# Kernel optimization log

Hardware: AMD Instinct MI355X
Metric: run time of the kernel (lower is better)

The kernel has to match this reference:

```python
import jax, jax.numpy as jnp
import numpy as np

B, S, HID, USZ, PSZ, OUT = 128, 512, 768, 200, 200, 200
N_SENT = 16  # 16 sentences of 32 tokens; offsets row = [0,32,...,480,-1]


def setup_inputs() -> dict:
    key = jax.random.key(0)
    ks = jax.random.split(key, 8)
    H = jax.random.normal(ks[0], (B, S, HID), jnp.float32)
    u = jax.random.normal(ks[1], (B, USZ), jnp.float32)
    p = jax.random.normal(ks[2], (B, PSZ), jnp.float32)
    Wh = jax.random.normal(ks[3], (HID, OUT), jnp.float32) * 0.05
    Wu = jax.random.normal(ks[4], (USZ, OUT), jnp.float32) * 0.05
    Wp = jax.random.normal(ks[5], (PSZ, OUT), jnp.float32) * 0.05
    v = jax.random.normal(ks[6], (OUT,), jnp.float32) * 0.05
    b = jnp.zeros((OUT,), jnp.float32)  # torch buffer self.b = zeros
    # offsets: N_SENT sentence starts + trailing -1 sentinel -> [B, N_SENT+1]
    row = jnp.concatenate([jnp.arange(N_SENT, dtype=jnp.int32) * (S // N_SENT),
                           jnp.array([-1], jnp.int32)])
    sentence_offsets = jnp.tile(row[None, :], (B, 1))
    return {"H": H, "u": u, "p": p, "Wh": Wh, "Wu": Wu, "Wp": Wp,
            "v": v, "b": b, "sentence_offsets": sentence_offsets}


def reference(H, u, p, Wh, Wu, Wp, v, b, sentence_offsets):
    # Additive attention scores for every token: v . tanh(Wh H + Wu u + Wp p + b)
    Ht = jnp.einsum('bsh,ho->bso', H, Wh)                      # [B,S,OUT]
    ut = (u @ Wu)[:, None, :]                                  # [B,1,OUT]
    pt = (p @ Wp)[:, None, :]                                  # [B,1,OUT]
    scores = jnp.tanh(Ht + ut + pt + b) @ v                    # [B,S]

    Bsz, Sl, _ = H.shape
    beg = sentence_offsets[:, :-1]                             # [B,M]
    nxt = sentence_offsets[:, 1:]                              # [B,M]
    valid = beg != -1
    # faithful to torch: end = 512 if next==-1 else next-1 (off-by-one kept)
    end = jnp.where(nxt == -1, Sl, nxt - 1)
    t = jnp.arange(Sl)
    mask = valid[:, :, None] & (t[None, None, :] >= beg[:, :, None]) \
           & (t[None, None, :] < end[:, :, None])              # [B,M,S]

    neg_inf = jnp.float32(-jnp.inf)
    em = jnp.where(mask, scores[:, None, :], neg_inf)
    m = jnp.max(em, axis=-1, keepdims=True)
    w = jnp.exp(em - jnp.where(jnp.isfinite(m), m, 0.0)) * mask
    denom = jnp.sum(w, axis=-1, keepdims=True)
    alphas = w / jnp.where(denom > 0, denom, 1.0)              # ragged softmax
    # per-sentence weighted sum of H -> [B, M, HID] (invalid sentences = 0)
    return jnp.einsum('bms,bsh->bmh', alphas, H)
```

## Files before the change

kernel.cpp:

```cpp
#include <hip/hip_runtime.h>
#include <hip/hip_bf16.h>
#include <math.h>

#define Bn   128
#define Sn   512
#define HIDn 768
#define OUTn 200
#define MSEG 16
#define NPAD 208
#define NT   13

typedef __attribute__((ext_vector_type(8))) short short8;
typedef __attribute__((ext_vector_type(4))) float f32x4;

static __device__ inline unsigned short f2bf(float f) {
  union { float f; unsigned u; } v; v.f = f;
  unsigned r = v.u + 0x7FFFu + ((v.u >> 16) & 1u);
  return (unsigned short)(r >> 16);
}

static __device__ inline float fast_tanh(float x) {
  float t = fabsf(x);
  float e = __expf(-2.f * t);
  float r = (1.f - e) * __builtin_amdgcn_rcpf(1.f + e);
  return copysignf(r, x);
}

__global__ __launch_bounds__(256) void setup_kernel(
    const float* __restrict__ Wh, const float* __restrict__ v,
    unsigned short* __restrict__ WhT, float* __restrict__ vP) {
  __shared__ float tile[16][17];
  int n0 = blockIdx.x * 16;
  int tid = threadIdx.x;
  if (blockIdx.x == 0 && tid < NPAD) vP[tid] = (tid < OUTn) ? v[tid] : 0.f;
  int tk = tid >> 4, tn = tid & 15;
  for (int k0 = 0; k0 < HIDn; k0 += 16) {
    float val = 0.f;
    int n = n0 + tn;
    if (n < OUTn) val = Wh[(size_t)(k0 + tk) * OUTn + n];
    tile[tk][tn] = val;
    __syncthreads();
    int tn2 = tid >> 4, tk2 = tid & 15;
    WhT[(size_t)(n0 + tn2) * HIDn + k0 + tk2] = f2bf(tile[tk2][tn2]);
    __syncthreads();
  }
}

__global__ __launch_bounds__(256) void bias_kernel(
    const float* __restrict__ u, const float* __restrict__ p,
    const float* __restrict__ Wu, const float* __restrict__ Wp,
    const float* __restrict__ bvec, float* __restrict__ biasP) {
  int b = blockIdx.x;
  __shared__ float ul[OUTn], pl[OUTn];
  int tid = threadIdx.x;
  if (tid < OUTn) { ul[tid] = u[b * OUTn + tid]; pl[tid] = p[b * OUTn + tid]; }
  __syncthreads();
  if (tid < NPAD) {
    float s = 0.f;
    if (tid < OUTn) {
      s = bvec[tid];
      for (int k = 0; k < OUTn; ++k)
        s += ul[k] * Wu[k * OUTn + tid] + pl[k] * Wp[k * OUTn + tid];
    }
    biasP[(size_t)b * NPAD + tid] = s;
  }
}

__global__ __launch_bounds__(256) void fused_kernel(
    const float* __restrict__ H, const unsigned short* __restrict__ WhT,
    const float* __restrict__ biasP, const float* __restrict__ vP,
    const int* __restrict__ offs, float* __restrict__ out) {
  __shared__ unsigned short Bl[NPAD * 32];
  __shared__ float al[128];
  int tid = threadIdx.x, wave = tid >> 6, lane = tid & 63;
  int quad = lane >> 4, l16 = lane & 15;
  int m0 = blockIdx.x * 128;
  int b = m0 >> 9;
  int s0 = m0 & 511;

  f32x4 acc[2][NT];
  for (int mt = 0; mt < 2; ++mt)
    for (int nt = 0; nt < NT; ++nt) acc[mt][nt] = (f32x4){0.f, 0.f, 0.f, 0.f};

  const float* Abase = H + (size_t)(m0 + wave * 32 + l16) * HIDn + quad * 8;

  for (int k0 = 0; k0 < HIDn; k0 += 32) {
    float4 f[2][2];
#pragma unroll
    for (int mt = 0; mt < 2; ++mt) {
      const float* ap = Abase + (size_t)mt * 16 * HIDn + k0;
      f[mt][0] = *(const float4*)ap;
      f[mt][1] = *(const float4*)(ap + 4);
    }
    __syncthreads();
    for (int i = tid; i < NPAD * 4; i += 256) {
      int n = i >> 2, c = i & 3;
      int4 d = *(const int4*)(WhT + (size_t)n * HIDn + k0 + c * 8);
      *(int4*)(&Bl[n * 32 + c * 8]) = d;
    }
    __syncthreads();

    short8 a[2];
#pragma unroll
    for (int mt = 0; mt < 2; ++mt) {
      short8 t;
      t[0] = f2bf(f[mt][0].x); t[1] = f2bf(f[mt][0].y);
      t[2] = f2bf(f[mt][0].z); t[3] = f2bf(f[mt][0].w);
      t[4] = f2bf(f[mt][1].x); t[5] = f2bf(f[mt][1].y);
      t[6] = f2bf(f[mt][1].z); t[7] = f2bf(f[mt][1].w);
      a[mt] = t;
    }
#pragma unroll
    for (int nt = 0; nt < NT; ++nt) {
      short8 bf = *(const short8*)(&Bl[(nt * 16 + l16) * 32 + quad * 8]);
      acc[0][nt] = __builtin_amdgcn_mfma_f32_16x16x32_bf16(a[0], bf, acc[0][nt], 0, 0, 0);
      acc[1][nt] = __builtin_amdgcn_mfma_f32_16x16x32_bf16(a[1], bf, acc[1][nt], 0, 0, 0);
    }
  }

  const float* bp = biasP + (size_t)b * NPAD;
  float sc[2][4];
#pragma unroll
  for (int mt = 0; mt < 2; ++mt) {
#pragma unroll
    for (int r = 0; r < 4; ++r) {
      float s = 0.f;
#pragma unroll
      for (int nt = 0; nt < NT; ++nt) {
        int n = nt * 16 + l16;
        s += fast_tanh(acc[mt][nt][r] + bp[n]) * vP[n];
      }
      s += __shfl_xor(s, 1); s += __shfl_xor(s, 2);
      s += __shfl_xor(s, 4); s += __shfl_xor(s, 8);
      sc[mt][r] = s;
    }
  }

  int seg = (s0 >> 5) + wave;
  int beg = offs[b * (MSEG + 1) + seg];
  int nxt = offs[b * (MSEG + 1) + seg + 1];
  bool valid = (beg != -1);
  int end = (nxt == -1) ? Sn : nxt - 1;

  float x[2][4];
  float mx = -INFINITY;
#pragma unroll
  for (int mt = 0; mt < 2; ++mt)
#pragma unroll
    for (int r = 0; r < 4; ++r) {
      int row = s0 + wave * 32 + mt * 16 + quad * 4 + r;
      bool in = valid && row >= beg && row < end;
      x[mt][r] = in ? sc[mt][r] : -INFINITY;
      mx = fmaxf(mx, x[mt][r]);
    }
  mx = fmaxf(mx, __shfl_xor(mx, 16));
  mx = fmaxf(mx, __shfl_xor(mx, 32));
  float mm = (mx > -1e30f) ? mx : 0.f;

  float e[2][4], ls = 0.f;
#pragma unroll
  for (int mt = 0; mt < 2; ++mt)
#pragma unroll
    for (int r = 0; r < 4; ++r) {
      e[mt][r] = __expf(x[mt][r] - mm);
      ls += e[mt][r];
    }
  ls += __shfl_xor(ls, 16);
  ls += __shfl_xor(ls, 32);
  float inv = (ls > 0.f) ? 1.f / ls : 0.f;

  if (l16 == 0) {
#pragma unroll
    for (int mt = 0; mt < 2; ++mt)
#pragma unroll
      for (int r = 0; r < 4; ++r)
        al[wave * 32 + mt * 16 + quad * 4 + r] = e[mt][r] * inv;
  }

  const float4* Hrow = (const float4*)(H + (size_t)(b * Sn + s0 + wave * 32) * HIDn);
  float4 o0 = {0,0,0,0}, o1 = {0,0,0,0}, o2 = {0,0,0,0};
  for (int i = 0; i < 32; ++i) {
    float a = al[wave * 32 + i];
    if (a != 0.f) {
      const float4* hp = Hrow + (size_t)i * (HIDn / 4);
      float4 h0 = hp[lane], h1 = hp[lane + 64], h2 = hp[lane + 128];
      o0.x += a * h0.x; o0.y += a * h0.y; o0.z += a * h0.z; o0.w += a * h0.w;
      o1.x += a * h1.x; o1.y += a * h1.y; o1.z += a * h1.z; o1.w += a * h1.w;
      o2.x += a * h2.x; o2.y += a * h2.y; o2.z += a * h2.z; o2.w += a * h2.w;
    }
  }
  float4* op = (float4*)(out + ((size_t)b * MSEG + seg) * HIDn);
  op[lane] = o0; op[lane + 64] = o1; op[lane + 128] = o2;
}

extern "C" void kernel_launch(void* const* d_in, const int* in_sizes, int n_in,
                              void* d_out, int out_size, void* d_ws, size_t ws_size,
                              hipStream_t stream) {
  const float* H    = (const float*)d_in[0];
  const float* u    = (const float*)d_in[1];
  const float* p    = (const float*)d_in[2];
  const float* Wh   = (const float*)d_in[3];
  const float* Wu   = (const float*)d_in[4];
  const float* Wp   = (const float*)d_in[5];
  const float* v    = (const float*)d_in[6];
  const float* bvec = (const float*)d_in[7];
  const int*   offs = (const int*)d_in[8];
  float* out = (float*)d_out;

  float* biasP = (float*)d_ws;
  float* vP    = biasP + (size_t)Bn * NPAD;
  unsigned short* WhT = (unsigned short*)(vP + NPAD);

  setup_kernel<<<NPAD / 16, 256, 0, stream>>>(Wh, v, WhT, vP);
  bias_kernel<<<Bn, 256, 0, stream>>>(u, p, Wu, Wp, bvec, biasP);
  fused_kernel<<<(Bn * Sn) / 128, 256, 0, stream>>>(H, WhT, biasP, vP, offs, out);
}
```

Measured before the change: 379.8 us.

## Load B fragments directly from global, parallelize setup transpose, split bias accumulation

The fused GEMM kernel no longer stages the bf16 Wh^T tile through LDS with two block barriers per k-step. Each lane now loads its B fragments straight from global memory (L2-resident) into registers. The setup transpose kernel is spread over 624 blocks, one 16x16 tile each, instead of 13 blocks looping over K. The bias kernel uses two partial sums to shorten its dependency chain. The direct loads add redundant global traffic per wave, since each of the four waves fetches the same B data, and 13 extra short8 registers per lane may add register pressure.

Measured after the change: 383.9 us. Within noise of the previous version (+1.1%).

```diff
diff --git a/kernel.cpp b/kernel.cpp
--- a/kernel.cpp
+++ b/kernel.cpp
@@ -30,20 +30,18 @@
     const float* __restrict__ Wh, const float* __restrict__ v,
     unsigned short* __restrict__ WhT, float* __restrict__ vP) {
   __shared__ float tile[16][17];
-  int n0 = blockIdx.x * 16;
+  int n0 = (blockIdx.x % 13) * 16;
+  int k0 = (blockIdx.x / 13) * 16;
   int tid = threadIdx.x;
   if (blockIdx.x == 0 && tid < NPAD) vP[tid] = (tid < OUTn) ? v[tid] : 0.f;
   int tk = tid >> 4, tn = tid & 15;
-  for (int k0 = 0; k0 < HIDn; k0 += 16) {
-    float val = 0.f;
-    int n = n0 + tn;
-    if (n < OUTn) val = Wh[(size_t)(k0 + tk) * OUTn + n];
-    tile[tk][tn] = val;
-    __syncthreads();
-    int tn2 = tid >> 4, tk2 = tid & 15;
-    WhT[(size_t)(n0 + tn2) * HIDn + k0 + tk2] = f2bf(tile[tk2][tn2]);
-    __syncthreads();
-  }
+  float val = 0.f;
+  int n = n0 + tn;
+  if (n < OUTn) val = Wh[(size_t)(k0 + tk) * OUTn + n];
+  tile[tk][tn] = val;
+  __syncthreads();
+  int tn2 = tid >> 4, tk2 = tid & 15;
+  WhT[(size_t)(n0 + tn2) * HIDn + k0 + tk2] = f2bf(tile[tk2][tn2]);
 }
 
 __global__ __launch_bounds__(256) void bias_kernel(
@@ -56,13 +54,15 @@
   if (tid < OUTn) { ul[tid] = u[b * OUTn + tid]; pl[tid] = p[b * OUTn + tid]; }
   __syncthreads();
   if (tid < NPAD) {
-    float s = 0.f;
+    float s0 = 0.f, s1 = 0.f;
     if (tid < OUTn) {
-      s = bvec[tid];
-      for (int k = 0; k < OUTn; ++k)
-        s += ul[k] * Wu[k * OUTn + tid] + pl[k] * Wp[k * OUTn + tid];
-    }
-    biasP[(size_t)b * NPAD + tid] = s;
+      s0 = bvec[tid];
+      for (int k = 0; k < OUTn; k += 2) {
+        s0 += ul[k] * Wu[k * OUTn + tid] + pl[k] * Wp[k * OUTn + tid];
+        s1 += ul[k + 1] * Wu[(k + 1) * OUTn + tid] + pl[k + 1] * Wp[(k + 1) * OUTn + tid];
+      }
+    }
+    biasP[(size_t)b * NPAD + tid] = s0 + s1;
   }
 }
 
@@ -70,7 +70,6 @@
     const float* __restrict__ H, const unsigned short* __restrict__ WhT,
     const float* __restrict__ biasP, const float* __restrict__ vP,
     const int* __restrict__ offs, float* __restrict__ out) {
-  __shared__ unsigned short Bl[NPAD * 32];
   __shared__ float al[128];
   int tid = threadIdx.x, wave = tid >> 6, lane = tid & 63;
   int quad = lane >> 4, l16 = lane & 15;
@@ -83,6 +82,7 @@
     for (int nt = 0; nt < NT; ++nt) acc[mt][nt] = (f32x4){0.f, 0.f, 0.f, 0.f};
 
   const float* Abase = H + (size_t)(m0 + wave * 32 + l16) * HIDn + quad * 8;
+  const unsigned short* Bbase = WhT + (size_t)l16 * HIDn + quad * 8;
 
   for (int k0 = 0; k0 < HIDn; k0 += 32) {
     float4 f[2][2];
@@ -92,13 +92,10 @@
       f[mt][0] = *(const float4*)ap;
       f[mt][1] = *(const float4*)(ap + 4);
     }
-    __syncthreads();
-    for (int i = tid; i < NPAD * 4; i += 256) {
-      int n = i >> 2, c = i & 3;
-      int4 d = *(const int4*)(WhT + (size_t)n * HIDn + k0 + c * 8);
-      *(int4*)(&Bl[n * 32 + c * 8]) = d;
-    }
-    __syncthreads();
+    short8 bfr[NT];
+#pragma unroll
+    for (int nt = 0; nt < NT; ++nt)
+      bfr[nt] = *(const short8*)(Bbase + (size_t)nt * 16 * HIDn + k0);
 
     short8 a[2];
 #pragma unroll
@@ -112,9 +109,8 @@
     }
 #pragma unroll
     for (int nt = 0; nt < NT; ++nt) {
-      short8 bf = *(const short8*)(&Bl[(nt * 16 + l16) * 32 + quad * 8]);
-      acc[0][nt] = __builtin_amdgcn_mfma_f32_16x16x32_bf16(a[0], bf, acc[0][nt], 0, 0, 0);
-      acc[1][nt] = __builtin_amdgcn_mfma_f32_16x16x32_bf16(a[1], bf, acc[1][nt], 0, 0, 0);
+      acc[0][nt] = __builtin_amdgcn_mfma_f32_16x16x32_bf16(a[0], bfr[nt], acc[0][nt], 0, 0, 0);
+      acc[1][nt] = __builtin_amdgcn_mfma_f32_16x16x32_bf16(a[1], bfr[nt], acc[1][nt], 0, 0, 0);
     }
   }
 
@@ -211,7 +207,7 @@
   float* vP    = biasP + (size_t)Bn * NPAD;
   unsigned short* WhT = (unsigned short*)(vP + NPAD);
 
-  setup_kernel<<<NPAD / 16, 256, 0, stream>>>(Wh, v, WhT, vP);
+  setup_kernel<<<13 * 48, 256, 0, stream>>>(Wh, v, WhT, vP);
   bias_kernel<<<Bn, 256, 0, stream>>>(u, p, Wu, Wp, bvec, biasP);
   fused_kernel<<<(Bn * Sn) / 128, 256, 0, stream>>>(H, WhT, biasP, vP, offs, out);
 }
```
